# Optimization experiments

Hardware: AMD Instinct MI355X
Metric: run time of the kernel (lower is better)

## Reference

```python
import jax, jax.numpy as jnp
import numpy as np

HEADS = 8
DIM_HEAD = 64
DIM = 512
KERNEL = 33
SCALE = DIM_HEAD ** -0.5


def setup_inputs() -> dict:
    key = jax.random.key(0)
    k1, k2, k3, k4, k5, k6 = jax.random.split(key, 6)
    b, n = 2, 2048
    inner = HEADS * DIM_HEAD
    x = jax.random.normal(k1, (b, n, DIM), dtype=jnp.float32)
    mask = jax.random.uniform(k2, (b, n)) < 0.9
    W_qkv = jax.random.normal(k3, (DIM, inner * 3), dtype=jnp.float32) / np.sqrt(DIM)
    W_out = jax.random.normal(k4, (inner, DIM), dtype=jnp.float32) / np.sqrt(inner)
    b_out = jax.random.normal(k5, (DIM,), dtype=jnp.float32) * 0.01
    # depthwise Conv2d(heads, heads, (K,1), groups=heads) weight: (O=heads, I/groups=1, K, 1)
    conv_w = jax.random.normal(k6, (HEADS, 1, KERNEL, 1), dtype=jnp.float32) / np.sqrt(KERNEL)
    return {"x": x, "mask": mask, "W_qkv": W_qkv, "W_out": W_out,
            "b_out": b_out, "conv_w": conv_w}


def reference(x, mask, W_qkv, W_out, b_out, conv_w):
    b, n, _ = x.shape
    h, d = HEADS, DIM_HEAD
    qkv = (x @ W_qkv).reshape(b, n, 3, h, d)          # chunk(3) then (h d) split
    q = qkv[:, :, 0].transpose(0, 2, 1, 3)            # b h n d
    k = qkv[:, :, 1].transpose(0, 2, 1, 3)
    v = qkv[:, :, 2].transpose(0, 2, 1, 3)
    dots = jnp.einsum('bhid,bhjd->bhij', q, k) * SCALE
    mask_value = -jnp.finfo(dots.dtype).max
    dots = jnp.where(mask[:, None, None, :], dots, mask_value)
    attn = jax.nn.softmax(dots, axis=-1)
    out = jnp.einsum('bhij,bhjd->bhid', attn, v)      # b h n d
    # depthwise residual conv over sequence axis (height), per head
    pad = KERNEL // 2
    res = jax.lax.conv_general_dilated(
        v, conv_w, window_strides=(1, 1), padding=((pad, pad), (0, 0)),
        dimension_numbers=('NCHW', 'OIHW', 'NCHW'), feature_group_count=h)
    out = out + res
    out = out.transpose(0, 2, 1, 3).reshape(b, n, h * d)  # b n (h d)
    out = out @ W_out + b_out
    out = jnp.where(mask[:, :, None], out, 0.0)
    return out
```

## Files before the change

### kernel.cpp

```cpp
#include <hip/hip_runtime.h>
#include <float.h>

#define BATCH 2
#define SEQ   2048
#define HEADS 8
#define DHEAD 64
#define DIMM  512
#define NQKV  1536
#define QSCALE_L2 (0.125f * 1.44269504f)

#define QKV_ELEMS ((size_t)BATCH * HEADS * SEQ * DHEAD)
#define BHS (BATCH * HEADS * SEQ)
#define NSPLIT 4

typedef __bf16 bf16x8 __attribute__((ext_vector_type(8)));
typedef short  s16x4  __attribute__((ext_vector_type(4)));
typedef float  f32x4  __attribute__((ext_vector_type(4)));

#if __has_builtin(__builtin_amdgcn_exp2f)
#define EXP2F __builtin_amdgcn_exp2f
#else
#define EXP2F exp2f
#endif

__device__ __forceinline__ unsigned short bfbits(float f) {
  __bf16 h = (__bf16)f;
  return *(unsigned short*)&h;
}
__device__ __forceinline__ float bf2f(unsigned short u) {
  return __uint_as_float((unsigned)u << 16);
}
__device__ __forceinline__ unsigned cvtpk(float a, float b) {
  unsigned r;
  asm("v_cvt_pk_bf16_f32 %0, %1, %2" : "=v"(r) : "v"(a), "v"(b));
  return r;
}
__device__ __forceinline__ f32x4 mfma16(s16x4 a, s16x4 b, f32x4 c) {
#if __has_builtin(__builtin_amdgcn_mfma_f32_16x16x16bf16_1k)
  return __builtin_amdgcn_mfma_f32_16x16x16bf16_1k(a, b, c, 0, 0, 0);
#else
  f32x4 d;
  asm("v_mfma_f32_16x16x16_bf16 %0, %1, %2, %3" : "=v"(d) : "v"(a), "v"(b), "v"(c));
  return d;
#endif
}

__device__ __forceinline__ void transpose_tile_dev(
    const float* __restrict__ W, unsigned short* __restrict__ Wt,
    int K, int N, int n0, int k0, int t, float T[64][65]) {
  {
    int r0 = t >> 4, c4 = t & 15;
#pragma unroll
    for (int rr = 0; rr < 4; ++rr) {
      int r = r0 + rr * 16;
      float4 v = *(const float4*)(W + (size_t)(k0 + r) * N + n0 + c4 * 4);
      T[r][c4 * 4 + 0] = v.x; T[r][c4 * 4 + 1] = v.y;
      T[r][c4 * 4 + 2] = v.z; T[r][c4 * 4 + 3] = v.w;
    }
  }
  __syncthreads();
  {
    int n = t >> 2, kc = t & 3;
    union { unsigned short u[16]; int4 v[2]; } p;
#pragma unroll
    for (int i = 0; i < 16; ++i) p.u[i] = bfbits(T[kc * 16 + i][n]);
    int4* dst = (int4*)(Wt + (size_t)(n0 + n) * K + k0 + kc * 16);
    dst[0] = p.v[0]; dst[1] = p.v[1];
  }
}

__global__ __launch_bounds__(256) void prep_all(
    const float* __restrict__ X, const void* __restrict__ mraw,
    const float* __restrict__ Wqkv, const float* __restrict__ Wout,
    unsigned short* __restrict__ Xbf, float* __restrict__ maskf,
    unsigned short* __restrict__ Wtq, unsigned short* __restrict__ Wto,
    unsigned* __restrict__ kmaxn) {
  __shared__ float T[64][65];
  __shared__ int f_bf16, f_f32, f_gt1, f_oddnz;
  const int b = blockIdx.x;
  const int t = threadIdx.x;
  if (b < 1024) {
    size_t i = ((size_t)b * 256 + t) * 8;
    float4 a0 = *(const float4*)(X + i);
    float4 a1 = *(const float4*)(X + i + 4);
    union { unsigned short u[8]; int4 v; } pk;
    pk.u[0] = bfbits(a0.x); pk.u[1] = bfbits(a0.y);
    pk.u[2] = bfbits(a0.z); pk.u[3] = bfbits(a0.w);
    pk.u[4] = bfbits(a1.x); pk.u[5] = bfbits(a1.y);
    pk.u[6] = bfbits(a1.z); pk.u[7] = bfbits(a1.w);
    *(int4*)(Xbf + i) = pk.v;
  } else if (b < 1216) {
    int bb2 = b - 1024;
    transpose_tile_dev(Wqkv, Wtq, DIMM, NQKV, (bb2 % 24) * 64, (bb2 / 24) * 64, t, T);
  } else if (b < 1280) {
    int bb2 = b - 1216;
    transpose_tile_dev(Wout, Wto, DIMM, DIMM, (bb2 & 7) * 64, (bb2 >> 3) * 64, t, T);
  } else {
    if (t < 16) kmaxn[t] = 0u;
    if (t == 0) { f_bf16 = 0; f_f32 = 0; f_gt1 = 0; f_oddnz = 0; }
    __syncthreads();
    const unsigned int* w = (const unsigned int*)mraw;
    unsigned int v = w[t];
    if (v == 0x3f803f80u) f_bf16 = 1;
    if (v == 0x3f800000u) f_f32 = 1;
    if (v > 1u)           f_gt1 = 1;
    if ((t & 1) && v != 0u) f_oddnz = 1;
    __syncthreads();
    int mode;
    if (f_bf16)       mode = 4;
    else if (f_f32)   mode = 3;
    else if (f_gt1)   mode = 1;
    else if (!f_oddnz) mode = 2;
    else              mode = 0;
    for (int i = t; i < BATCH * SEQ; i += 256) {
      bool keep;
      if (mode == 4)      keep = ((const unsigned short*)mraw)[i] != 0;
      else if (mode == 3) keep = ((const float*)mraw)[i] != 0.f;
      else if (mode == 1) keep = ((const unsigned char*)mraw)[i] != 0;
      else if (mode == 2) keep = w[2 * i] != 0u;
      else                keep = w[i] != 0u;
      maskf[i] = keep ? 1.f : 0.f;
    }
  }
}

__global__ __launch_bounds__(256) void gemm_qkv_mfma(
    const unsigned short* __restrict__ Xbf, const unsigned short* __restrict__ Wt,
    unsigned short* __restrict__ Qbf, unsigned short* __restrict__ Kbf,
    unsigned short* __restrict__ Vt, unsigned* __restrict__ kmaxn) {
  __shared__ __align__(16) unsigned char Al[128 * 128];
  __shared__ __align__(16) unsigned char Bl[64 * 128];
  const int tid = threadIdx.x;
  const int lane = tid & 63;
  const int w = tid >> 6;
  const int l15 = lane & 15, g = lane >> 4;
  const int wr = w >> 1, wc = w & 1;
  int bid = blockIdx.x;
  int lid = (bid & 7) * 96 + (bid >> 3);
  int by = lid / 24, bx = lid - by * 24;
  const int m0 = by * 128;

  f32x4 acc[4][2] = {};
  const int srow = tid >> 3, scg = tid & 7;
  const int rsw = (l15 & 7) << 4;

  for (int k0 = 0; k0 < DIMM; k0 += 64) {
    __syncthreads();
#pragma unroll
    for (int it = 0; it < 4; ++it) {
      int row = srow + it * 32;
      int sw = (row & 7) << 4;
      *(int4*)(Al + row * 128 + ((scg * 16) ^ sw)) =
          *(const int4*)(Xbf + (size_t)(m0 + row) * DIMM + k0 + scg * 8);
      if (it < 2) {
        *(int4*)(Bl + row * 128 + ((scg * 16) ^ sw)) =
            *(const int4*)(Wt + (size_t)(bx * 64 + row) * DIMM + k0 + scg * 8);
      }
    }
    __syncthreads();
#pragma unroll
    for (int ks = 0; ks < 2; ++ks) {
      bf16x8 af[4], bfr[2];
#pragma unroll
      for (int mi = 0; mi < 4; ++mi)
        af[mi] = *(const bf16x8*)(Al + (wr * 64 + mi * 16 + l15) * 128 +
                                  ((ks * 64 + g * 16) ^ rsw));
#pragma unroll
      for (int nj = 0; nj < 2; ++nj)
        bfr[nj] = *(const bf16x8*)(Bl + (wc * 32 + nj * 16 + l15) * 128 +
                                   ((ks * 64 + g * 16) ^ rsw));
#pragma unroll
      for (int mi = 0; mi < 4; ++mi)
#pragma unroll
        for (int nj = 0; nj < 2; ++nj)
          acc[mi][nj] = __builtin_amdgcn_mfma_f32_16x16x32_bf16(
              af[mi], bfr[nj], acc[mi][nj], 0, 0, 0);
    }
  }
  const int chunk = bx >> 3;
  const int bb = m0 >> 11;
  const int hh = bx & 7;
  if (chunk == 2) {
#pragma unroll
    for (int nj = 0; nj < 2; ++nj) {
      int dd = wc * 32 + nj * 16 + l15;
#pragma unroll
      for (int mi = 0; mi < 4; ++mi) {
        int ii0 = (m0 & (SEQ - 1)) + wr * 64 + mi * 16 + g * 4;
        union { unsigned short u[4]; ushort4 v; } pk;
#pragma unroll
        for (int r = 0; r < 4; ++r) pk.u[r] = bfbits(acc[mi][nj][r]);
        *(ushort4*)(Vt + ((size_t)(bb * HEADS + hh) * DHEAD + dd) * SEQ + ii0) = pk.v;
      }
    }
  } else {
    if (chunk == 1) {
      float kab = 0.f;
#pragma unroll
      for (int nj = 0; nj < 2; ++nj)
#pragma unroll
        for (int mi = 0; mi < 4; ++mi)
#pragma unroll
          for (int r = 0; r < 4; ++r) kab = fmaxf(kab, fabsf(acc[mi][nj][r]));
#pragma unroll
      for (int d = 1; d < 64; d <<= 1) kab = fmaxf(kab, __shfl_xor(kab, d));
      if (lane == 0)
        atomicMax(kmaxn + (bb * HEADS + hh), __float_as_uint(kab * 1.005f));
    }
    unsigned short* dst = (chunk == 0) ? Qbf : Kbf;
    const float sc = (chunk == 0) ? QSCALE_L2 : 1.f;
    __syncthreads();
#pragma unroll
    for (int nj = 0; nj < 2; ++nj) {
      int dd = wc * 32 + nj * 16 + l15;
#pragma unroll
      for (int mi = 0; mi < 4; ++mi) {
#pragma unroll
        for (int r = 0; r < 4; ++r) {
          int rowl = wr * 64 + mi * 16 + g * 4 + r;
          *(unsigned short*)(Al + rowl * 128 + ((dd * 2) ^ ((rowl & 7) << 4))) =
              bfbits(acc[mi][nj][r] * sc);
        }
      }
    }
    __syncthreads();
    const int rr = tid >> 1, hf = tid & 1;
    const int ii0 = (m0 & (SEQ - 1));
    unsigned short* gout =
        dst + ((size_t)(bb * HEADS + hh) * SEQ + ii0 + rr) * DHEAD + hf * 32;
    const int sw2 = (rr & 7) << 4;
#pragma unroll
    for (int q = 0; q < 4; ++q)
      *(int4*)(gout + q * 8) =
          *(const int4*)(Al + rr * 128 + ((hf * 64 + q * 16) ^ sw2));
  }
}

__global__ __launch_bounds__(256) void attn_split(const unsigned short* __restrict__ Qbf,
                                                  const unsigned short* __restrict__ Kbf,
                                                  const unsigned short* __restrict__ Vt,
                                                  const float* __restrict__ maskf,
                                                  const unsigned* __restrict__ kmaxn,
                                                  unsigned short* __restrict__ Po,
                                                  float* __restrict__ LSUM) {
  __shared__ __align__(16) unsigned char Ks[16384];
  __shared__ __align__(16) unsigned char Vs[16384];

  const int tid = threadIdx.x;
  const int lane = tid & 63;
  const int w = tid >> 6;
  const int l15 = lane & 15, g = lane >> 4;

  int fid = blockIdx.x;
  int lid = (fid & 7) * 256 + (fid >> 3);
  const int bh = lid >> 7;
  const int rem = lid & 127;
  const int qb = rem >> 2;
  const int quarter = rem & 3;
  const int bb = bh >> 3;

  const unsigned short* Qg = Qbf + ((size_t)bh * SEQ + qb * 64) * DHEAD;
  const unsigned short* Kg = Kbf + (size_t)bh * SEQ * DHEAD;
  const unsigned short* Vg = Vt  + (size_t)bh * DHEAD * SEQ;
  const float* mrow = maskf + bb * SEQ;

  bf16x8 qf0, qf1;
  {
    const unsigned char* qrow = (const unsigned char*)(Qg + (size_t)(w * 16 + l15) * DHEAD);
    qf0 = *(const bf16x8*)(qrow + g * 16);
    qf1 = *(const bf16x8*)(qrow + 64 + g * 16);
  }
  float Bx;
  {
    float qn2 = 0.f;
#pragma unroll
    for (int i = 0; i < 8; ++i) {
      float a = (float)qf0[i]; qn2 += a * a;
      float b = (float)qf1[i]; qn2 += b * b;
    }
    qn2 += __shfl_xor(qn2, 16);
    qn2 += __shfl_xor(qn2, 32);
    const float kabs = __uint_as_float(kmaxn[bh]);
    Bx = sqrtf(qn2) * 8.f * kabs;
  }

  f32x4 o[4] = {};
  float lsum = 0.f;

  const int sm = tid >> 2;
  const int sc = (tid & 3) * 32;
  const int ssw = (sm & 7) << 4;
  const int vswap = (sm >> 3) & 1;
  const int rsw = (l15 & 7) << 4;
  const int vsw = rsw | (((l15 >> 3) & 1) << 3);
  const int kt0 = quarter * 8;

  int4 rk0, rk1, rv0, rv1;
  {
    const unsigned char* ksrc =
        (const unsigned char*)(Kg + (size_t)kt0 * 64 * DHEAD) + sm * 128 + sc;
    const unsigned char* vsrc =
        (const unsigned char*)(Vg + (size_t)sm * SEQ + kt0 * 64) + sc;
    rk0 = *(const int4*)(ksrc); rk1 = *(const int4*)(ksrc + 16);
    rv0 = *(const int4*)(vsrc); rv1 = *(const int4*)(vsrc + 16);
  }
  {
    *(int4*)(Ks + sm * 128 + ((sc)      ^ ssw)) = rk0;
    *(int4*)(Ks + sm * 128 + ((sc + 16) ^ ssw)) = rk1;
    int4 sv0 = vswap ? (int4){rv0.z, rv0.w, rv0.x, rv0.y} : rv0;
    int4 sv1 = vswap ? (int4){rv1.z, rv1.w, rv1.x, rv1.y} : rv1;
    *(int4*)(Vs + sm * 128 + ((sc)      ^ ssw)) = sv0;
    *(int4*)(Vs + sm * 128 + ((sc + 16) ^ ssw)) = sv1;
  }
  __syncthreads();

  for (int t = 0; t < 8; ++t) {
    const int kt = kt0 + t;
    const int co = (t & 1) << 13;
    const int no = co ^ 8192;
    float4 km[4];
#pragma unroll
    for (int j = 0; j < 4; ++j) km[j] = *(const float4*)(mrow + kt * 64 + 16 * j + 4 * g);
    if (t < 7) {
      const unsigned char* ksrc =
          (const unsigned char*)(Kg + (size_t)(kt + 1) * 64 * DHEAD) + sm * 128 + sc;
      const unsigned char* vsrc =
          (const unsigned char*)(Vg + (size_t)sm * SEQ + (kt + 1) * 64) + sc;
      rk0 = *(const int4*)(ksrc); rk1 = *(const int4*)(ksrc + 16);
      rv0 = *(const int4*)(vsrc); rv1 = *(const int4*)(vsrc + 16);
    }

    f32x4 s[4];
#pragma unroll
    for (int j = 0; j < 4; ++j) {
      const unsigned char* krow = Ks + co + (16 * j + l15) * 128;
      bf16x8 kf0 = *(const bf16x8*)(krow + ((g * 16)      ^ rsw));
      bf16x8 kf1 = *(const bf16x8*)(krow + ((64 + g * 16) ^ rsw));
      f32x4 z = (f32x4){0.f, 0.f, 0.f, 0.f};
      z = __builtin_amdgcn_mfma_f32_16x16x32_bf16(kf0, qf0, z, 0, 0, 0);
      z = __builtin_amdgcn_mfma_f32_16x16x32_bf16(kf1, qf1, z, 0, 0, 0);
      s[j] = z;
    }

    s16x4 pa[4];
#pragma unroll
    for (int j = 0; j < 4; ++j) {
      float p0 = EXP2F(s[j][0] - Bx) * km[j].x;
      float p1 = EXP2F(s[j][1] - Bx) * km[j].y;
      float p2 = EXP2F(s[j][2] - Bx) * km[j].z;
      float p3 = EXP2F(s[j][3] - Bx) * km[j].w;
      lsum += (p0 + p1) + (p2 + p3);
      union { uint2 u; s16x4 v; } pk;
      pk.u.x = cvtpk(p0, p1);
      pk.u.y = cvtpk(p2, p3);
      pa[j] = pk.v;
    }

#pragma unroll
    for (int dj = 0; dj < 4; ++dj) {
      const unsigned char* vrow = Vs + co + (16 * dj + l15) * 128;
#pragma unroll
      for (int j = 0; j < 4; ++j) {
        s16x4 vb = *(const s16x4*)(vrow + ((32 * j + 8 * g) ^ vsw));
        o[dj] = mfma16(pa[j], vb, o[dj]);
      }
    }

    if (t < 7) {
      *(int4*)(Ks + no + sm * 128 + ((sc)      ^ ssw)) = rk0;
      *(int4*)(Ks + no + sm * 128 + ((sc + 16) ^ ssw)) = rk1;
      int4 sv0 = vswap ? (int4){rv0.z, rv0.w, rv0.x, rv0.y} : rv0;
      int4 sv1 = vswap ? (int4){rv1.z, rv1.w, rv1.x, rv1.y} : rv1;
      *(int4*)(Vs + no + sm * 128 + ((sc)      ^ ssw)) = sv0;
      *(int4*)(Vs + no + sm * 128 + ((sc + 16) ^ ssw)) = sv1;
      __syncthreads();
    }
  }

#pragma unroll
  for (int r = 0; r < 4; ++r) {
    int row = qb * 64 + w * 16 + 4 * g + r;
    size_t base = (size_t)quarter * QKV_ELEMS + ((size_t)bh * SEQ + row) * DHEAD + l15;
    Po[base]      = bfbits(o[0][r]);
    Po[base + 16] = bfbits(o[1][r]);
    Po[base + 32] = bfbits(o[2][r]);
    Po[base + 48] = bfbits(o[3][r]);
  }
  lsum += __shfl_xor(lsum, 16);
  lsum += __shfl_xor(lsum, 32);
  if (g == 0) {
    int row = qb * 64 + w * 16 + l15;
    LSUM[quarter * BHS + bh * SEQ + row] = lsum;
  }
}

__global__ __launch_bounds__(256) void combine_conv(
    const unsigned short* __restrict__ Po, const float* __restrict__ LSUM,
    const unsigned short* __restrict__ Vt, const float* __restrict__ cw,
    unsigned short* __restrict__ Obf) {
  __shared__ float T[96][68];
  __shared__ float cwl[33];
  const int tid = threadIdx.x;
  const int bid = blockIdx.x;
  const int bh = bid >> 5;
  const int n0 = (bid & 31) * 64;
  const int hh = bh & 7;
  if (tid < 33) cwl[tid] = cw[hh * 33 + tid];
  for (int idx = tid; idx < 64 * 24; idx += 256) {
    int d = idx / 24, c4 = idx - (idx / 24) * 24;
    int nbase = n0 - 16 + c4 * 4;
    const unsigned short* src = Vt + ((size_t)bh * DHEAD + d) * SEQ;
#pragma unroll
    for (int q = 0; q < 4; ++q) {
      int n = nbase + q;
      T[c4 * 4 + q][d] = (n >= 0 && n < SEQ) ? bf2f(src[n]) : 0.f;
    }
  }
  __syncthreads();
#pragma unroll
  for (int p = 0; p < 4; ++p) {
    int n = (tid >> 4) + p * 16;
    int d4 = tid & 15;
    int row = bh * SEQ + n0 + n;
    float tot = 0.f;
#pragma unroll
    for (int q = 0; q < NSPLIT; ++q) tot += LSUM[q * BHS + row];
    float inv = (tot > 0.f) ? 1.f / tot : 0.f;
    float o0 = 0.f, o1 = 0.f, o2 = 0.f, o3 = 0.f;
#pragma unroll
    for (int q = 0; q < NSPLIT; ++q) {
      ushort4 a = *(const ushort4*)(Po + (size_t)q * QKV_ELEMS + (size_t)row * DHEAD + d4 * 4);
      o0 += bf2f(a.x); o1 += bf2f(a.y);
      o2 += bf2f(a.z); o3 += bf2f(a.w);
    }
    o0 *= inv; o1 *= inv; o2 *= inv; o3 *= inv;
#pragma unroll
    for (int t = 0; t < 33; ++t) {
      float wv = cwl[t];
      float4 tv = *(const float4*)&T[n + t][d4 * 4];
      o0 += wv * tv.x; o1 += wv * tv.y; o2 += wv * tv.z; o3 += wv * tv.w;
    }
    union { unsigned short u[4]; ushort4 v; } pk;
    pk.u[0] = bfbits(o0); pk.u[1] = bfbits(o1);
    pk.u[2] = bfbits(o2); pk.u[3] = bfbits(o3);
    *(ushort4*)(Obf + (size_t)row * DHEAD + d4 * 4) = pk.v;
  }
}

__global__ __launch_bounds__(256) void gemm_out_mfma(
    const unsigned short* __restrict__ Obf, const unsigned short* __restrict__ Wt,
    const float* __restrict__ bias, const float* __restrict__ maskf,
    float* __restrict__ out) {
  __shared__ __align__(16) unsigned char Al[64 * 128];
  __shared__ __align__(16) unsigned char Bl[64 * 128];
  const int tid = threadIdx.x;
  const int lane = tid & 63;
  const int w = tid >> 6;
  const int l15 = lane & 15, g = lane >> 4;
  const int wr = w >> 1, wc = w & 1;
  int bid = blockIdx.x;
  int lid = (bid & 7) * 64 + (bid >> 3);
  int by = lid >> 3, bx = lid & 7;
  const int m0 = by * 64, n0 = bx * 64;
  const int bb = m0 >> 11;
  const int ii0 = m0 & (SEQ - 1);

  f32x4 acc[2][2] = {};
  const int srow = tid >> 3, scg = tid & 7;
  const int rsw = (l15 & 7) << 4;

  for (int k0 = 0; k0 < DIMM; k0 += 64) {
    const int hh = k0 >> 6;
    __syncthreads();
#pragma unroll
    for (int it = 0; it < 2; ++it) {
      int row = srow + it * 32;
      int sw = (row & 7) << 4;
      *(int4*)(Al + row * 128 + ((scg * 16) ^ sw)) =
          *(const int4*)(Obf + ((size_t)(bb * HEADS + hh) * SEQ + ii0 + row) * DHEAD + scg * 8);
      *(int4*)(Bl + row * 128 + ((scg * 16) ^ sw)) =
          *(const int4*)(Wt + (size_t)(n0 + row) * DIMM + k0 + scg * 8);
    }
    __syncthreads();
#pragma unroll
    for (int ks = 0; ks < 2; ++ks) {
      bf16x8 af[2], bfr[2];
#pragma unroll
      for (int mi = 0; mi < 2; ++mi)
        af[mi] = *(const bf16x8*)(Al + (wr * 32 + mi * 16 + l15) * 128 +
                                  ((ks * 64 + g * 16) ^ rsw));
#pragma unroll
      for (int nj = 0; nj < 2; ++nj)
        bfr[nj] = *(const bf16x8*)(Bl + (wc * 32 + nj * 16 + l15) * 128 +
                                   ((ks * 64 + g * 16) ^ rsw));
#pragma unroll
      for (int mi = 0; mi < 2; ++mi)
#pragma unroll
        for (int nj = 0; nj < 2; ++nj)
          acc[mi][nj] = __builtin_amdgcn_mfma_f32_16x16x32_bf16(
              af[mi], bfr[nj], acc[mi][nj], 0, 0, 0);
    }
  }
#pragma unroll
  for (int nj = 0; nj < 2; ++nj) {
    int col = n0 + wc * 32 + nj * 16 + l15;
    float bcol = bias[col];
#pragma unroll
    for (int mi = 0; mi < 2; ++mi) {
#pragma unroll
      for (int r = 0; r < 4; ++r) {
        int m = m0 + wr * 32 + mi * 16 + g * 4 + r;
        out[(size_t)m * DIMM + col] = (acc[mi][nj][r] + bcol) * maskf[m];
      }
    }
  }
}

extern "C" void kernel_launch(void* const* d_in, const int* in_sizes, int n_in,
                              void* d_out, int out_size, void* d_ws, size_t ws_size,
                              hipStream_t stream) {
  const float* x     = (const float*)d_in[0];
  const void*  mask  = d_in[1];
  const float* Wqkv  = (const float*)d_in[2];
  const float* Wout  = (const float*)d_in[3];
  const float* bout  = (const float*)d_in[4];
  const float* convw = (const float*)d_in[5];
  float* out = (float*)d_out;

  float* maskf = (float*)d_ws;
  unsigned* kmaxn = (unsigned*)(maskf + 4096);
  unsigned short* Qbf = (unsigned short*)(kmaxn + 64);
  unsigned short* Kbf = Qbf + QKV_ELEMS;
  unsigned short* Vt  = Kbf + QKV_ELEMS;
  unsigned short* Po  = Vt + QKV_ELEMS;
  float* LSUM         = (float*)(Po + NSPLIT * QKV_ELEMS);
  unsigned short* Obf = (unsigned short*)(LSUM + NSPLIT * BHS);
  unsigned short* Wtq = Obf + QKV_ELEMS;
  unsigned short* Wto = Wtq + (size_t)NQKV * DIMM;
  unsigned short* Xbf = Wto + (size_t)DIMM * DIMM;

  prep_all<<<1281, 256, 0, stream>>>(x, mask, Wqkv, Wout, Xbf, maskf, Wtq, Wto, kmaxn);
  gemm_qkv_mfma<<<768, 256, 0, stream>>>(Xbf, Wtq, Qbf, Kbf, Vt, kmaxn);
  attn_split<<<2048, 256, 0, stream>>>(Qbf, Kbf, Vt, maskf, kmaxn, Po, LSUM);
  combine_conv<<<512, 256, 0, stream>>>(Po, LSUM, Vt, convw, Obf);
  gemm_out_mfma<<<512, 256, 0, stream>>>(Obf, Wto, bout, maskf, out);
}
```

Measured before the change: 99.00 us.

## Process two query tiles per attention block to reuse staged K/V tiles

Each attention block now handles 128 query rows, as two 64-row sub-tiles sharing every K/V tile loaded into shared memory, and the grid is halved to 1024 blocks. This halves global K/V traffic and LDS staging per query row, and amortizes barriers across twice the MFMA work. It also adds s_setprio around the MFMA sections to favor matrix issue. The cost is more accumulator registers, which may lower occupancy, and fewer blocks to spread over the CUs.

```diff
diff --git a/kernel.cpp b/kernel.cpp
--- a/kernel.cpp
+++ b/kernel.cpp
@@ -252,40 +252,46 @@
   const int l15 = lane & 15, g = lane >> 4;
 
   int fid = blockIdx.x;
-  int lid = (fid & 7) * 256 + (fid >> 3);
-  const int bh = lid >> 7;
-  const int rem = lid & 127;
-  const int qb = rem >> 2;
+  int lid = (fid & 7) * 128 + (fid >> 3);
+  const int bh = lid >> 6;
+  const int rem = lid & 63;
+  const int qp = rem >> 2;
   const int quarter = rem & 3;
   const int bb = bh >> 3;
 
-  const unsigned short* Qg = Qbf + ((size_t)bh * SEQ + qb * 64) * DHEAD;
+  const unsigned short* Qg = Qbf + ((size_t)bh * SEQ + qp * 128) * DHEAD;
   const unsigned short* Kg = Kbf + (size_t)bh * SEQ * DHEAD;
   const unsigned short* Vg = Vt  + (size_t)bh * DHEAD * SEQ;
   const float* mrow = maskf + bb * SEQ;
 
-  bf16x8 qf0, qf1;
+  bf16x8 qf0a, qf1a, qf0b, qf1b;
   {
-    const unsigned char* qrow = (const unsigned char*)(Qg + (size_t)(w * 16 + l15) * DHEAD);
-    qf0 = *(const bf16x8*)(qrow + g * 16);
-    qf1 = *(const bf16x8*)(qrow + 64 + g * 16);
-  }
-  float Bx;
+    const unsigned char* qra = (const unsigned char*)(Qg + (size_t)(w * 16 + l15) * DHEAD);
+    qf0a = *(const bf16x8*)(qra + g * 16);
+    qf1a = *(const bf16x8*)(qra + 64 + g * 16);
+    const unsigned char* qrb = qra + 64 * DHEAD * 2;
+    qf0b = *(const bf16x8*)(qrb + g * 16);
+    qf1b = *(const bf16x8*)(qrb + 64 + g * 16);
+  }
+  float Bxa, Bxb;
   {
-    float qn2 = 0.f;
+    const float kabs = __uint_as_float(kmaxn[bh]);
+    float qa = 0.f, qb2 = 0.f;
 #pragma unroll
     for (int i = 0; i < 8; ++i) {
-      float a = (float)qf0[i]; qn2 += a * a;
-      float b = (float)qf1[i]; qn2 += b * b;
-    }
-    qn2 += __shfl_xor(qn2, 16);
-    qn2 += __shfl_xor(qn2, 32);
-    const float kabs = __uint_as_float(kmaxn[bh]);
-    Bx = sqrtf(qn2) * 8.f * kabs;
-  }
-
-  f32x4 o[4] = {};
-  float lsum = 0.f;
+      float a0 = (float)qf0a[i]; qa += a0 * a0;
+      float a1 = (float)qf1a[i]; qa += a1 * a1;
+      float b0 = (float)qf0b[i]; qb2 += b0 * b0;
+      float b1 = (float)qf1b[i]; qb2 += b1 * b1;
+    }
+    qa += __shfl_xor(qa, 16);  qa += __shfl_xor(qa, 32);
+    qb2 += __shfl_xor(qb2, 16); qb2 += __shfl_xor(qb2, 32);
+    Bxa = sqrtf(qa) * 8.f * kabs;
+    Bxb = sqrtf(qb2) * 8.f * kabs;
+  }
+
+  f32x4 oa[4] = {}, ob[4] = {};
+  float lsa = 0.f, lsb = 0.f;
 
   const int sm = tid >> 2;
   const int sc = (tid & 3) * 32;
@@ -330,41 +336,57 @@
       rv0 = *(const int4*)(vsrc); rv1 = *(const int4*)(vsrc + 16);
     }
 
-    f32x4 s[4];
+    f32x4 sa[4], sb[4];
+    __builtin_amdgcn_s_setprio(1);
 #pragma unroll
     for (int j = 0; j < 4; ++j) {
       const unsigned char* krow = Ks + co + (16 * j + l15) * 128;
       bf16x8 kf0 = *(const bf16x8*)(krow + ((g * 16)      ^ rsw));
       bf16x8 kf1 = *(const bf16x8*)(krow + ((64 + g * 16) ^ rsw));
-      f32x4 z = (f32x4){0.f, 0.f, 0.f, 0.f};
-      z = __builtin_amdgcn_mfma_f32_16x16x32_bf16(kf0, qf0, z, 0, 0, 0);
-      z = __builtin_amdgcn_mfma_f32_16x16x32_bf16(kf1, qf1, z, 0, 0, 0);
-      s[j] = z;
-    }
-
-    s16x4 pa[4];
+      f32x4 za = (f32x4){0.f, 0.f, 0.f, 0.f};
+      za = __builtin_amdgcn_mfma_f32_16x16x32_bf16(kf0, qf0a, za, 0, 0, 0);
+      za = __builtin_amdgcn_mfma_f32_16x16x32_bf16(kf1, qf1a, za, 0, 0, 0);
+      sa[j] = za;
+      f32x4 zb = (f32x4){0.f, 0.f, 0.f, 0.f};
+      zb = __builtin_amdgcn_mfma_f32_16x16x32_bf16(kf0, qf0b, zb, 0, 0, 0);
+      zb = __builtin_amdgcn_mfma_f32_16x16x32_bf16(kf1, qf1b, zb, 0, 0, 0);
+      sb[j] = zb;
+    }
+    __builtin_amdgcn_s_setprio(0);
+
+    s16x4 paA[4], paB[4];
 #pragma unroll
     for (int j = 0; j < 4; ++j) {
-      float p0 = EXP2F(s[j][0] - Bx) * km[j].x;
-      float p1 = EXP2F(s[j][1] - Bx) * km[j].y;
-      float p2 = EXP2F(s[j][2] - Bx) * km[j].z;
-      float p3 = EXP2F(s[j][3] - Bx) * km[j].w;
-      lsum += (p0 + p1) + (p2 + p3);
+      float a0 = EXP2F(sa[j][0] - Bxa) * km[j].x;
+      float a1 = EXP2F(sa[j][1] - Bxa) * km[j].y;
+      float a2 = EXP2F(sa[j][2] - Bxa) * km[j].z;
+      float a3 = EXP2F(sa[j][3] - Bxa) * km[j].w;
+      lsa += (a0 + a1) + (a2 + a3);
       union { uint2 u; s16x4 v; } pk;
-      pk.u.x = cvtpk(p0, p1);
-      pk.u.y = cvtpk(p2, p3);
-      pa[j] = pk.v;
-    }
-
+      pk.u.x = cvtpk(a0, a1); pk.u.y = cvtpk(a2, a3);
+      paA[j] = pk.v;
+      float b0 = EXP2F(sb[j][0] - Bxb) * km[j].x;
+      float b1 = EXP2F(sb[j][1] - Bxb) * km[j].y;
+      float b2 = EXP2F(sb[j][2] - Bxb) * km[j].z;
+      float b3 = EXP2F(sb[j][3] - Bxb) * km[j].w;
+      lsb += (b0 + b1) + (b2 + b3);
+      union { uint2 u; s16x4 v; } pk2;
+      pk2.u.x = cvtpk(b0, b1); pk2.u.y = cvtpk(b2, b3);
+      paB[j] = pk2.v;
+    }
+
+    __builtin_amdgcn_s_setprio(1);
 #pragma unroll
     for (int dj = 0; dj < 4; ++dj) {
       const unsigned char* vrow = Vs + co + (16 * dj + l15) * 128;
 #pragma unroll
       for (int j = 0; j < 4; ++j) {
         s16x4 vb = *(const s16x4*)(vrow + ((32 * j + 8 * g) ^ vsw));
-        o[dj] = mfma16(pa[j], vb, o[dj]);
+        oa[dj] = mfma16(paA[j], vb, oa[dj]);
+        ob[dj] = mfma16(paB[j], vb, ob[dj]);
       }
     }
+    __builtin_amdgcn_s_setprio(0);
 
     if (t < 7) {
       *(int4*)(Ks + no + sm * 128 + ((sc)      ^ ssw)) = rk0;
@@ -379,18 +401,24 @@
 
 #pragma unroll
   for (int r = 0; r < 4; ++r) {
-    int row = qb * 64 + w * 16 + 4 * g + r;
-    size_t base = (size_t)quarter * QKV_ELEMS + ((size_t)bh * SEQ + row) * DHEAD + l15;
-    Po[base]      = bfbits(o[0][r]);
-    Po[base + 16] = bfbits(o[1][r]);
-    Po[base + 32] = bfbits(o[2][r]);
-    Po[base + 48] = bfbits(o[3][r]);
-  }
-  lsum += __shfl_xor(lsum, 16);
-  lsum += __shfl_xor(lsum, 32);
+    int rowa = qp * 128 + w * 16 + 4 * g + r;
+    size_t basea = (size_t)quarter * QKV_ELEMS + ((size_t)bh * SEQ + rowa) * DHEAD + l15;
+    Po[basea]      = bfbits(oa[0][r]);
+    Po[basea + 16] = bfbits(oa[1][r]);
+    Po[basea + 32] = bfbits(oa[2][r]);
+    Po[basea + 48] = bfbits(oa[3][r]);
+    size_t baseb = basea + (size_t)64 * DHEAD;
+    Po[baseb]      = bfbits(ob[0][r]);
+    Po[baseb + 16] = bfbits(ob[1][r]);
+    Po[baseb + 32] = bfbits(ob[2][r]);
+    Po[baseb + 48] = bfbits(ob[3][r]);
+  }
+  lsa += __shfl_xor(lsa, 16); lsa += __shfl_xor(lsa, 32);
+  lsb += __shfl_xor(lsb, 16); lsb += __shfl_xor(lsb, 32);
   if (g == 0) {
-    int row = qb * 64 + w * 16 + l15;
-    LSUM[quarter * BHS + bh * SEQ + row] = lsum;
+    int rowa = qp * 128 + w * 16 + l15;
+    LSUM[quarter * BHS + bh * SEQ + rowa] = lsa;
+    LSUM[quarter * BHS + bh * SEQ + rowa + 64] = lsb;
   }
 }
 
@@ -541,7 +569,7 @@
 
   prep_all<<<1281, 256, 0, stream>>>(x, mask, Wqkv, Wout, Xbf, maskf, Wtq, Wto, kmaxn);
   gemm_qkv_mfma<<<768, 256, 0, stream>>>(Xbf, Wtq, Qbf, Kbf, Vt, kmaxn);
-  attn_split<<<2048, 256, 0, stream>>>(Qbf, Kbf, Vt, maskf, kmaxn, Po, LSUM);
+  attn_split<<<1024, 256, 0, stream>>>(Qbf, Kbf, Vt, maskf, kmaxn, Po, LSUM);
   combine_conv<<<512, 256, 0, stream>>>(Po, LSUM, Vt, convw, Obf);
   gemm_out_mfma<<<512, 256, 0, stream>>>(Obf, Wto, bout, maskf, out);
 }
```

After: 99.45 us. Within noise of the previous version (+0.5%).
